# Kernel tuning notes

Hardware: AMD Instinct MI355X
Metric: run time of the kernel (lower is better)

## Reference

```python
import jax, jax.numpy as jnp
import numpy as np

B, S, D = 4, 2048, 1024


def setup_inputs() -> dict:
    key = jax.random.key(0)
    ks = jax.random.split(key, 4)
    scale = 1.0 / np.sqrt(D)
    x = jax.random.normal(ks[0], (B, S, D), dtype=jnp.float32)
    Wk = jax.random.normal(ks[1], (D, D), dtype=jnp.float32) * scale
    Wq = jax.random.normal(ks[2], (D, D), dtype=jnp.float32) * scale
    Wv = jax.random.normal(ks[3], (D, D), dtype=jnp.float32) * scale
    bk = jnp.zeros((D,), dtype=jnp.float32)
    bq = jnp.zeros((D,), dtype=jnp.float32)
    bv = jnp.zeros((D,), dtype=jnp.float32)
    return {"x": x, "Wk": Wk, "bk": bk, "Wq": Wq, "bq": bq,
            "Wv": Wv, "bv": bv, "dims": 2}


def correlated_weight(k, q, v, dims):
    # correlation between every query position and every key position,
    # scaled by sqrt(d) for numerical stability (standard correlation attn)
    d = q.shape[-1]
    scores = jnp.einsum("bqd,bkd->bqk", q, k) / jnp.sqrt(jnp.asarray(d, q.dtype))
    w = jax.nn.softmax(scores, axis=dims)          # [B, S, S]
    return jnp.einsum("bqk,bkd->bqd", w, v)        # [B, S, D]


def reference(x, Wk, bk, Wq, bq, Wv, bv, dims):
    # injected key/query/value funcs instantiated as Linear layers
    k = jnp.einsum("bsd,de->bse", x, Wk) + bk
    q = jnp.einsum("bsd,de->bse", x, Wq) + bq
    v = jnp.einsum("bsd,de->bse", x, Wv) + bv
    return correlated_weight(k, q, v, dims)
```

## Files before the change

kernel.cpp:

```cpp
#include <hip/hip_runtime.h>
#include <hip/hip_bf16.h>
#include <stdint.h>


typedef unsigned short u16;
typedef __bf16 bf16x8 __attribute__((ext_vector_type(8)));
typedef float  f32x16 __attribute__((ext_vector_type(16)));
typedef u16    u16x4  __attribute__((ext_vector_type(4)));
typedef u16    u16x8  __attribute__((ext_vector_type(8)));

__device__ __forceinline__ u16 f2bf(float f) {
  union { float f; uint32_t u; } v; v.f = f;
  uint32_t r = v.u + 0x7fffu + ((v.u >> 16) & 1u);
  return (u16)(r >> 16);
}

#define GLD_LDS16(gp, lp) __builtin_amdgcn_global_load_lds(                   \
    (const __attribute__((address_space(1))) void*)(gp),                      \
    (__attribute__((address_space(3))) void*)(lp), 16, 0, 0)


__global__ __launch_bounds__(256) void conv_x(const float* __restrict__ in,
                                              u16* __restrict__ out, int n) {
  int i = (blockIdx.x * 256 + threadIdx.x) * 4;
  if (i >= n) return;
  float4 v = *(const float4*)(in + i);
  u16x4 o; o.x = f2bf(v.x); o.y = f2bf(v.y); o.z = f2bf(v.z); o.w = f2bf(v.w);
  *(u16x4*)(out + i) = o;
}

__global__ __launch_bounds__(256) void trans_conv_w(const float* __restrict__ W,
                                                    u16* __restrict__ Wt) {
  __shared__ float t[32][33];
  int e0 = blockIdx.x * 32, d0 = blockIdx.y * 32;
  #pragma unroll
  for (int i = 0; i < 4; ++i)
    t[threadIdx.y + i * 8][threadIdx.x] =
        W[(size_t)(d0 + threadIdx.y + i * 8) * 1024 + e0 + threadIdx.x];
  __syncthreads();
  #pragma unroll
  for (int i = 0; i < 4; ++i)
    Wt[(size_t)(e0 + threadIdx.y + i * 8) * 1024 + d0 + threadIdx.x] =
        f2bf(t[threadIdx.x][threadIdx.y + i * 8]);
}

__global__ __launch_bounds__(256) void concat_bias(const float* __restrict__ bq,
                                                   const float* __restrict__ bk,
                                                   const float* __restrict__ bv,
                                                   float* __restrict__ bc) {
  int i = blockIdx.x * 256 + threadIdx.x;
  if (i >= 3072) return;
  bc[i] = (i < 1024) ? bq[i] : (i < 2048 ? bk[i - 1024] : bv[i - 2048]);
}

__global__ __launch_bounds__(256) void trans_v(const u16* __restrict__ qkv,
                                               u16* __restrict__ vT) {
  __shared__ u16 t[32][33];
  int b = blockIdx.z;
  int s0 = blockIdx.x * 32, e0 = blockIdx.y * 32;
  const u16* src = qkv + (size_t)b * 2048 * 3072 + 2048;
  u16* dst = vT + (size_t)b * 1024 * 2048;
  #pragma unroll
  for (int i = 0; i < 4; ++i)
    t[threadIdx.y + i * 8][threadIdx.x] =
        src[(size_t)(s0 + threadIdx.y + i * 8) * 3072 + e0 + threadIdx.x];
  __syncthreads();
  #pragma unroll
  for (int i = 0; i < 4; ++i)
    dst[(size_t)(e0 + threadIdx.y + i * 8) * 2048 + s0 + threadIdx.x] =
        t[threadIdx.x][threadIdx.y + i * 8];
}


template <bool OUT_BF16, bool BIAS>
__global__ __launch_bounds__(256)
void gemm_bt(const u16* __restrict__ A, int lda, long long sA,
             const u16* __restrict__ B, int ldb, long long sB,
             void* __restrict__ C, int ldc, long long sC,
             const float* __restrict__ bias, int K, float scale) {
  __shared__ u16 As[128 * 64];
  __shared__ u16 Bs[128 * 64];
  const int lane = threadIdx.x & 63;
  const int wv = threadIdx.x >> 6;

  const u16* Ab = A + (size_t)blockIdx.z * sA + (size_t)blockIdx.y * 128 * lda;
  const u16* Bb = B + (size_t)blockIdx.z * sB + (size_t)blockIdx.x * 128 * ldb;

  const int srow = lane >> 3;
  const int scol = ((lane & 7) ^ (lane >> 3)) * 8;
  const int r32 = lane & 31;
  const int half = lane >> 5;
  const int rx = lane & 7;
  const int wm = (wv >> 1) * 64;
  const int wn = (wv & 1) * 64;

  f32x16 acc[2][2];
  #pragma unroll
  for (int i = 0; i < 2; ++i)
    #pragma unroll
    for (int j = 0; j < 2; ++j) acc[i][j] = (f32x16)0.0f;

  for (int k0 = 0; k0 < K; k0 += 64) {
    #pragma unroll
    for (int i = 0; i < 4; ++i) {
      int r = wv * 32 + i * 8;
      GLD_LDS16(Ab + (size_t)(r + srow) * lda + k0 + scol, As + r * 64);
      GLD_LDS16(Bb + (size_t)(r + srow) * ldb + k0 + scol, Bs + r * 64);
    }
    __syncthreads();

    bf16x8 af[2][4], bfr[2][4];
    #pragma unroll
    for (int i = 0; i < 2; ++i)
      #pragma unroll
      for (int t = 0; t < 4; ++t) {
        int pc = ((t * 2 + half) ^ rx) * 8;
        af[i][t]  = *(const bf16x8*)(As + (wm + i * 32 + r32) * 64 + pc);
        bfr[i][t] = *(const bf16x8*)(Bs + (wn + i * 32 + r32) * 64 + pc);
      }
    #pragma unroll
    for (int i = 0; i < 2; ++i)
      #pragma unroll
      for (int j = 0; j < 2; ++j)
        #pragma unroll
        for (int t = 0; t < 4; ++t)
          acc[i][j] = __builtin_amdgcn_mfma_f32_32x32x16_bf16(
              af[i][t], bfr[j][t], acc[i][j], 0, 0, 0);
    __syncthreads();
  }

  const int ccol0 = blockIdx.x * 128 + wn + r32;
  const int crow0 = blockIdx.y * 128 + wm + 4 * half;
  u16* Cb = (u16*)C + (size_t)blockIdx.z * sC;
  float* Cf = (float*)C + (size_t)blockIdx.z * sC;
  #pragma unroll
  for (int i = 0; i < 2; ++i) {
    #pragma unroll
    for (int e = 0; e < 16; ++e) {
      int m = crow0 + i * 32 + (e & 3) + 8 * (e >> 2);
      #pragma unroll
      for (int j = 0; j < 2; ++j) {
        int n = ccol0 + j * 32;
        float v = acc[i][j][e] * scale;
        if (BIAS) v += bias[n];
        if (OUT_BF16) Cb[(size_t)m * ldc + n] = f2bf(v);
        else          Cf[(size_t)m * ldc + n] = v;
      }
    }
  }
}


__global__ __launch_bounds__(256) void softmax_rows(float* __restrict__ S) {
  __shared__ float red[4];
  const int t = threadIdx.x;
  const int lane = t & 63, wv = t >> 6;
  float* row = S + (size_t)blockIdx.x * 2048;
  const float4* rv = (const float4*)row;
  float4 a = rv[t * 2], b = rv[t * 2 + 1];
  float v[8] = {a.x, a.y, a.z, a.w, b.x, b.y, b.z, b.w};
  float m = v[0];
  #pragma unroll
  for (int j = 1; j < 8; ++j) m = fmaxf(m, v[j]);
  #pragma unroll
  for (int off = 32; off > 0; off >>= 1) m = fmaxf(m, __shfl_down(m, off));
  if (lane == 0) red[wv] = m;
  __syncthreads();
  m = fmaxf(fmaxf(red[0], red[1]), fmaxf(red[2], red[3]));
  __syncthreads();
  float e[8], s = 0.f;
  #pragma unroll
  for (int j = 0; j < 8; ++j) { e[j] = exp2f((v[j] - m) * 1.44269504f); s += e[j]; }
  #pragma unroll
  for (int off = 32; off > 0; off >>= 1) s += __shfl_down(s, off);
  if (lane == 0) red[wv] = s;
  __syncthreads();
  s = red[0] + red[1] + red[2] + red[3];
  float inv = 1.0f / s;
  u16x8 w;
  #pragma unroll
  for (int j = 0; j < 8; ++j) w[j] = f2bf(e[j] * inv);
  ((u16x8*)row)[t] = w;
}


extern "C" void kernel_launch(void* const* d_in, const int* in_sizes, int n_in,
                              void* d_out, int out_size, void* d_ws, size_t ws_size,
                              hipStream_t stream) {
  const float* x  = (const float*)d_in[0];
  const float* Wk = (const float*)d_in[1];
  const float* bk = (const float*)d_in[2];
  const float* Wq = (const float*)d_in[3];
  const float* bq = (const float*)d_in[4];
  const float* Wv = (const float*)d_in[5];
  const float* bv = (const float*)d_in[6];
  float* out = (float*)d_out;

  char* ws = (char*)d_ws;
  u16*   xb  = (u16*)(ws + 0);
  u16*   wt  = (u16*)(ws + 16777216);
  float* bc  = (float*)(ws + 23068672);
  u16*   qkv = (u16*)(ws + 23080960);
  u16*   vT  = (u16*)(ws + 73412608);
  float* sc  = (float*)(ws + 90189824);
  (void)in_sizes; (void)n_in; (void)out_size; (void)ws_size;

  conv_x<<<8192, 256, 0, stream>>>(x, xb, 8388608);
  trans_conv_w<<<dim3(32, 32), dim3(32, 8), 0, stream>>>(Wq, wt);
  trans_conv_w<<<dim3(32, 32), dim3(32, 8), 0, stream>>>(Wk, wt + 1024 * 1024);
  trans_conv_w<<<dim3(32, 32), dim3(32, 8), 0, stream>>>(Wv, wt + 2 * 1024 * 1024);
  concat_bias<<<12, 256, 0, stream>>>(bq, bk, bv, bc);

  gemm_bt<true, true><<<dim3(24, 64, 1), 256, 0, stream>>>(
      xb, 1024, 0LL, wt, 1024, 0LL, (void*)qkv, 3072, 0LL, bc, 1024, 1.0f);

  trans_v<<<dim3(64, 32, 4), dim3(32, 8), 0, stream>>>(qkv, vT);

  gemm_bt<false, false><<<dim3(16, 16, 4), 256, 0, stream>>>(
      qkv, 3072, 2048LL * 3072, qkv + 1024, 3072, 2048LL * 3072,
      (void*)sc, 2048, 2048LL * 2048, nullptr, 1024, 0.03125f);

  softmax_rows<<<8192, 256, 0, stream>>>(sc);

  gemm_bt<false, false><<<dim3(8, 16, 4), 256, 0, stream>>>(
      (const u16*)sc, 4096, 2048LL * 4096, vT, 2048, 1024LL * 2048,
      (void*)out, 1024, 2048LL * 1024, nullptr, 2048, 1.0f);
}
```

Before: 288.0 us.

## Store scores as bf16, vectorize V transpose, merge weight transposes, 8-wave PV GEMM

The QK^T GEMM now writes bf16 scores instead of fp32, so softmax reads and writes half the bytes in place. The V transpose uses 64x64 tiles with 16-byte vector loads and stores. The three weight transposes are merged into one launch. The PV GEMM uses a new 512-thread kernel so more waves cover each tile. Rounding scores to bf16 before softmax costs some accuracy.

```diff
diff --git a/kernel.cpp b/kernel.cpp
--- a/kernel.cpp
+++ b/kernel.cpp
@@ -13,6 +13,9 @@
   union { float f; uint32_t u; } v; v.f = f;
   uint32_t r = v.u + 0x7fffu + ((v.u >> 16) & 1u);
   return (u16)(r >> 16);
+}
+__device__ __forceinline__ float bf2f(u16 b) {
+  union { uint32_t u; float f; } v; v.u = (uint32_t)b << 16; return v.f;
 }
 
 #define GLD_LDS16(gp, lp) __builtin_amdgcn_global_load_lds(                   \
@@ -29,9 +32,13 @@
   *(u16x4*)(out + i) = o;
 }
 
-__global__ __launch_bounds__(256) void trans_conv_w(const float* __restrict__ W,
-                                                    u16* __restrict__ Wt) {
+__global__ __launch_bounds__(256) void trans_conv_w3(const float* __restrict__ Wq,
+                                                     const float* __restrict__ Wk,
+                                                     const float* __restrict__ Wv,
+                                                     u16* __restrict__ Wt) {
   __shared__ float t[32][33];
+  const float* W = blockIdx.z == 0 ? Wq : (blockIdx.z == 1 ? Wk : Wv);
+  u16* dst = Wt + (size_t)blockIdx.z * 1024 * 1024;
   int e0 = blockIdx.x * 32, d0 = blockIdx.y * 32;
   #pragma unroll
   for (int i = 0; i < 4; ++i)
@@ -40,7 +47,7 @@
   __syncthreads();
   #pragma unroll
   for (int i = 0; i < 4; ++i)
-    Wt[(size_t)(e0 + threadIdx.y + i * 8) * 1024 + d0 + threadIdx.x] =
+    dst[(size_t)(e0 + threadIdx.y + i * 8) * 1024 + d0 + threadIdx.x] =
         f2bf(t[threadIdx.x][threadIdx.y + i * 8]);
 }
 
@@ -55,20 +62,25 @@
 
 __global__ __launch_bounds__(256) void trans_v(const u16* __restrict__ qkv,
                                                u16* __restrict__ vT) {
-  __shared__ u16 t[32][33];
+  __shared__ u16 t[64][72];
   int b = blockIdx.z;
-  int s0 = blockIdx.x * 32, e0 = blockIdx.y * 32;
+  int s0 = blockIdx.x * 64, e0 = blockIdx.y * 64;
   const u16* src = qkv + (size_t)b * 2048 * 3072 + 2048;
   u16* dst = vT + (size_t)b * 1024 * 2048;
-  #pragma unroll
-  for (int i = 0; i < 4; ++i)
-    t[threadIdx.y + i * 8][threadIdx.x] =
-        src[(size_t)(s0 + threadIdx.y + i * 8) * 3072 + e0 + threadIdx.x];
-  __syncthreads();
-  #pragma unroll
-  for (int i = 0; i < 4; ++i)
-    dst[(size_t)(e0 + threadIdx.y + i * 8) * 2048 + s0 + threadIdx.x] =
-        t[threadIdx.x][threadIdx.y + i * 8];
+  int tx = threadIdx.x & 7, ty = threadIdx.x >> 3;
+  #pragma unroll
+  for (int rr = 0; rr < 64; rr += 32)
+    *(u16x8*)&t[ty + rr][tx * 8] =
+        *(const u16x8*)(src + (size_t)(s0 + ty + rr) * 3072 + e0 + tx * 8);
+  __syncthreads();
+  #pragma unroll
+  for (int rr = 0; rr < 64; rr += 32) {
+    int er = ty + rr;
+    u16x8 o;
+    #pragma unroll
+    for (int j = 0; j < 8; ++j) o[j] = t[tx * 8 + j][er];
+    *(u16x8*)(dst + (size_t)(e0 + er) * 2048 + s0 + tx * 8) = o;
+  }
 }
 
 
@@ -150,15 +162,78 @@
   }
 }
 
-
-__global__ __launch_bounds__(256) void softmax_rows(float* __restrict__ S) {
+__global__ __launch_bounds__(512)
+void gemm_bt8(const u16* __restrict__ A, int lda, long long sA,
+              const u16* __restrict__ B, int ldb, long long sB,
+              float* __restrict__ C, int ldc, long long sC,
+              int K, float scale) {
+  __shared__ u16 As[128 * 64];
+  __shared__ u16 Bs[128 * 64];
+  const int lane = threadIdx.x & 63;
+  const int wv = threadIdx.x >> 6;
+
+  const u16* Ab = A + (size_t)blockIdx.z * sA + (size_t)blockIdx.y * 128 * lda;
+  const u16* Bb = B + (size_t)blockIdx.z * sB + (size_t)blockIdx.x * 128 * ldb;
+
+  const int srow = lane >> 3;
+  const int scol = ((lane & 7) ^ (lane >> 3)) * 8;
+  const int r32 = lane & 31;
+  const int half = lane >> 5;
+  const int rx = lane & 7;
+  const int wm = (wv >> 2) * 64;
+  const int wn = (wv & 3) * 32;
+
+  f32x16 acc[2];
+  acc[0] = (f32x16)0.0f; acc[1] = (f32x16)0.0f;
+
+  for (int k0 = 0; k0 < K; k0 += 64) {
+    #pragma unroll
+    for (int i = 0; i < 2; ++i) {
+      int r = wv * 16 + i * 8;
+      GLD_LDS16(Ab + (size_t)(r + srow) * lda + k0 + scol, As + r * 64);
+      GLD_LDS16(Bb + (size_t)(r + srow) * ldb + k0 + scol, Bs + r * 64);
+    }
+    __syncthreads();
+
+    bf16x8 af[2][4], bfr[4];
+    #pragma unroll
+    for (int t = 0; t < 4; ++t) {
+      int pc = ((t * 2 + half) ^ rx) * 8;
+      af[0][t] = *(const bf16x8*)(As + (wm + r32) * 64 + pc);
+      af[1][t] = *(const bf16x8*)(As + (wm + 32 + r32) * 64 + pc);
+      bfr[t]   = *(const bf16x8*)(Bs + (wn + r32) * 64 + pc);
+    }
+    #pragma unroll
+    for (int i = 0; i < 2; ++i)
+      #pragma unroll
+      for (int t = 0; t < 4; ++t)
+        acc[i] = __builtin_amdgcn_mfma_f32_32x32x16_bf16(
+            af[i][t], bfr[t], acc[i], 0, 0, 0);
+    __syncthreads();
+  }
+
+  const int ccol = blockIdx.x * 128 + wn + r32;
+  const int crow0 = blockIdx.y * 128 + wm + 4 * half;
+  float* Cf = C + (size_t)blockIdx.z * sC;
+  #pragma unroll
+  for (int i = 0; i < 2; ++i)
+    #pragma unroll
+    for (int e = 0; e < 16; ++e) {
+      int m = crow0 + i * 32 + (e & 3) + 8 * (e >> 2);
+      Cf[(size_t)m * ldc + ccol] = acc[i][e] * scale;
+    }
+}
+
+
+__global__ __launch_bounds__(256) void softmax_rows(u16* __restrict__ P) {
   __shared__ float red[4];
   const int t = threadIdx.x;
   const int lane = t & 63, wv = t >> 6;
-  float* row = S + (size_t)blockIdx.x * 2048;
-  const float4* rv = (const float4*)row;
-  float4 a = rv[t * 2], b = rv[t * 2 + 1];
-  float v[8] = {a.x, a.y, a.z, a.w, b.x, b.y, b.z, b.w};
+  u16* row = P + (size_t)blockIdx.x * 2048;
+  u16x8 w = ((const u16x8*)row)[t];
+  float v[8];
+  #pragma unroll
+  for (int j = 0; j < 8; ++j) v[j] = bf2f(w[j]);
   float m = v[0];
   #pragma unroll
   for (int j = 1; j < 8; ++j) m = fmaxf(m, v[j]);
@@ -177,10 +252,10 @@
   __syncthreads();
   s = red[0] + red[1] + red[2] + red[3];
   float inv = 1.0f / s;
-  u16x8 w;
-  #pragma unroll
-  for (int j = 0; j < 8; ++j) w[j] = f2bf(e[j] * inv);
-  ((u16x8*)row)[t] = w;
+  u16x8 o;
+  #pragma unroll
+  for (int j = 0; j < 8; ++j) o[j] = f2bf(e[j] * inv);
+  ((u16x8*)row)[t] = o;
 }
 
 
@@ -202,27 +277,25 @@
   float* bc  = (float*)(ws + 23068672);
   u16*   qkv = (u16*)(ws + 23080960);
   u16*   vT  = (u16*)(ws + 73412608);
-  float* sc  = (float*)(ws + 90189824);
+  u16*   P   = (u16*)(ws + 90189824);
   (void)in_sizes; (void)n_in; (void)out_size; (void)ws_size;
 
   conv_x<<<8192, 256, 0, stream>>>(x, xb, 8388608);
-  trans_conv_w<<<dim3(32, 32), dim3(32, 8), 0, stream>>>(Wq, wt);
-  trans_conv_w<<<dim3(32, 32), dim3(32, 8), 0, stream>>>(Wk, wt + 1024 * 1024);
-  trans_conv_w<<<dim3(32, 32), dim3(32, 8), 0, stream>>>(Wv, wt + 2 * 1024 * 1024);
+  trans_conv_w3<<<dim3(32, 32, 3), dim3(32, 8), 0, stream>>>(Wq, Wk, Wv, wt);
   concat_bias<<<12, 256, 0, stream>>>(bq, bk, bv, bc);
 
   gemm_bt<true, true><<<dim3(24, 64, 1), 256, 0, stream>>>(
       xb, 1024, 0LL, wt, 1024, 0LL, (void*)qkv, 3072, 0LL, bc, 1024, 1.0f);
 
-  trans_v<<<dim3(64, 32, 4), dim3(32, 8), 0, stream>>>(qkv, vT);
-
-  gemm_bt<false, false><<<dim3(16, 16, 4), 256, 0, stream>>>(
+  trans_v<<<dim3(32, 16, 4), 256, 0, stream>>>(qkv, vT);
+
+  gemm_bt<true, false><<<dim3(16, 16, 4), 256, 0, stream>>>(
       qkv, 3072, 2048LL * 3072, qkv + 1024, 3072, 2048LL * 3072,
-      (void*)sc, 2048, 2048LL * 2048, nullptr, 1024, 0.03125f);
-
-  softmax_rows<<<8192, 256, 0, stream>>>(sc);
-
-  gemm_bt<false, false><<<dim3(8, 16, 4), 256, 0, stream>>>(
-      (const u16*)sc, 4096, 2048LL * 4096, vT, 2048, 1024LL * 2048,
-      (void*)out, 1024, 2048LL * 1024, nullptr, 2048, 1.0f);
-}
+      (void*)P, 2048, 2048LL * 2048, nullptr, 1024, 0.03125f);
+
+  softmax_rows<<<8192, 256, 0, stream>>>(P);
+
+  gemm_bt8<<<dim3(8, 16, 4), 512, 0, stream>>>(
+      P, 2048, 2048LL * 2048, vT, 2048, 1024LL * 2048,
+      out, 1024, 2048LL * 1024, 2048, 1.0f);
+}
```

After: 275.5 us. 4.3% less time.

## Fuse exp into score GEMM, drop max, defer normalization, switch to 16x16 MFMA

Applied to the files above, without the earlier changes.

The score GEMM now applies exp2 in its epilogue and writes bf16 probabilities directly, without subtracting the row max. A small rowsum kernel computes the normalizers, and the PV GEMM divides by them in its epilogue. This replaces the fp32 score matrix and the full softmax pass. The change also moves all GEMMs from 32x32 to 16x16 MFMA tiles, uses a BN=64 tile for the output GEMM, merges the three weight-transpose launches into one, and vectorizes the V transpose. Skipping the max subtraction risks overflow for large scores, and exp values are rounded to bf16 before they are summed.

```diff
diff --git a/kernel.cpp b/kernel.cpp
--- a/kernel.cpp
+++ b/kernel.cpp
@@ -5,7 +5,7 @@
 
 typedef unsigned short u16;
 typedef __bf16 bf16x8 __attribute__((ext_vector_type(8)));
-typedef float  f32x16 __attribute__((ext_vector_type(16)));
+typedef float  f32x4  __attribute__((ext_vector_type(4)));
 typedef u16    u16x4  __attribute__((ext_vector_type(4)));
 typedef u16    u16x8  __attribute__((ext_vector_type(8)));
 
@@ -13,6 +13,9 @@
   union { float f; uint32_t u; } v; v.f = f;
   uint32_t r = v.u + 0x7fffu + ((v.u >> 16) & 1u);
   return (u16)(r >> 16);
+}
+__device__ __forceinline__ float bf2f(u16 b) {
+  union { uint32_t u; float f; } v; v.u = (uint32_t)b << 16; return v.f;
 }
 
 #define GLD_LDS16(gp, lp) __builtin_amdgcn_global_load_lds(                   \
@@ -29,9 +32,13 @@
   *(u16x4*)(out + i) = o;
 }
 
-__global__ __launch_bounds__(256) void trans_conv_w(const float* __restrict__ W,
-                                                    u16* __restrict__ Wt) {
+__global__ __launch_bounds__(256) void trans_conv_w3(const float* __restrict__ Wq,
+                                                     const float* __restrict__ Wk,
+                                                     const float* __restrict__ Wv,
+                                                     u16* __restrict__ Wt) {
   __shared__ float t[32][33];
+  const float* W = blockIdx.z == 0 ? Wq : (blockIdx.z == 1 ? Wk : Wv);
+  u16* dst = Wt + (size_t)blockIdx.z * 1024 * 1024;
   int e0 = blockIdx.x * 32, d0 = blockIdx.y * 32;
   #pragma unroll
   for (int i = 0; i < 4; ++i)
@@ -40,7 +47,7 @@
   __syncthreads();
   #pragma unroll
   for (int i = 0; i < 4; ++i)
-    Wt[(size_t)(e0 + threadIdx.y + i * 8) * 1024 + d0 + threadIdx.x] =
+    dst[(size_t)(e0 + threadIdx.y + i * 8) * 1024 + d0 + threadIdx.x] =
         f2bf(t[threadIdx.x][threadIdx.y + i * 8]);
 }
 
@@ -55,94 +62,117 @@
 
 __global__ __launch_bounds__(256) void trans_v(const u16* __restrict__ qkv,
                                                u16* __restrict__ vT) {
-  __shared__ u16 t[32][33];
+  __shared__ u16 t[64][72];
   int b = blockIdx.z;
-  int s0 = blockIdx.x * 32, e0 = blockIdx.y * 32;
+  int s0 = blockIdx.x * 64, e0 = blockIdx.y * 64;
   const u16* src = qkv + (size_t)b * 2048 * 3072 + 2048;
   u16* dst = vT + (size_t)b * 1024 * 2048;
-  #pragma unroll
-  for (int i = 0; i < 4; ++i)
-    t[threadIdx.y + i * 8][threadIdx.x] =
-        src[(size_t)(s0 + threadIdx.y + i * 8) * 3072 + e0 + threadIdx.x];
+  int tx = threadIdx.x & 7, ty = threadIdx.x >> 3;
+  #pragma unroll
+  for (int rr = 0; rr < 64; rr += 32)
+    *(u16x8*)&t[ty + rr][tx * 8] =
+        *(const u16x8*)(src + (size_t)(s0 + ty + rr) * 3072 + e0 + tx * 8);
   __syncthreads();
   #pragma unroll
-  for (int i = 0; i < 4; ++i)
-    dst[(size_t)(e0 + threadIdx.y + i * 8) * 2048 + s0 + threadIdx.x] =
-        t[threadIdx.x][threadIdx.y + i * 8];
-}
-
-
-template <bool OUT_BF16, bool BIAS>
+  for (int rr = 0; rr < 64; rr += 32) {
+    int er = ty + rr;
+    u16x8 o;
+    #pragma unroll
+    for (int j = 0; j < 8; ++j) o[j] = t[tx * 8 + j][er];
+    *(u16x8*)(dst + (size_t)(e0 + er) * 2048 + s0 + tx * 8) = o;
+  }
+}
+
+
+template <int BN, bool OUT_BF16, bool BIAS, bool EXP, bool DIV>
 __global__ __launch_bounds__(256)
-void gemm_bt(const u16* __restrict__ A, int lda, long long sA,
-             const u16* __restrict__ B, int ldb, long long sB,
-             void* __restrict__ C, int ldc, long long sC,
-             const float* __restrict__ bias, int K, float scale) {
+void gemm16(const u16* __restrict__ A, int lda, long long sA,
+            const u16* __restrict__ B, int ldb, long long sB,
+            void* __restrict__ C, int ldc, long long sC,
+            const float* __restrict__ aux, int K, float scale) {
+  constexpr int NJ = BN / 32;
   __shared__ u16 As[128 * 64];
-  __shared__ u16 Bs[128 * 64];
+  __shared__ u16 Bs[BN * 64];
   const int lane = threadIdx.x & 63;
   const int wv = threadIdx.x >> 6;
 
   const u16* Ab = A + (size_t)blockIdx.z * sA + (size_t)blockIdx.y * 128 * lda;
-  const u16* Bb = B + (size_t)blockIdx.z * sB + (size_t)blockIdx.x * 128 * ldb;
+  const u16* Bb = B + (size_t)blockIdx.z * sB + (size_t)blockIdx.x * BN * ldb;
 
   const int srow = lane >> 3;
   const int scol = ((lane & 7) ^ (lane >> 3)) * 8;
-  const int r32 = lane & 31;
-  const int half = lane >> 5;
+  const int row16 = lane & 15;
+  const int quad = lane >> 4;
   const int rx = lane & 7;
   const int wm = (wv >> 1) * 64;
-  const int wn = (wv & 1) * 64;
-
-  f32x16 acc[2][2];
-  #pragma unroll
-  for (int i = 0; i < 2; ++i)
-    #pragma unroll
-    for (int j = 0; j < 2; ++j) acc[i][j] = (f32x16)0.0f;
+  const int wn = (wv & 1) * (BN / 2);
+
+  f32x4 acc[4][NJ];
+  #pragma unroll
+  for (int i = 0; i < 4; ++i)
+    #pragma unroll
+    for (int j = 0; j < NJ; ++j) acc[i][j] = (f32x4)0.0f;
 
   for (int k0 = 0; k0 < K; k0 += 64) {
     #pragma unroll
     for (int i = 0; i < 4; ++i) {
       int r = wv * 32 + i * 8;
       GLD_LDS16(Ab + (size_t)(r + srow) * lda + k0 + scol, As + r * 64);
+    }
+    #pragma unroll
+    for (int i = 0; i < BN / 32; ++i) {
+      int r = wv * (BN / 4) + i * 8;
       GLD_LDS16(Bb + (size_t)(r + srow) * ldb + k0 + scol, Bs + r * 64);
     }
     __syncthreads();
 
-    bf16x8 af[2][4], bfr[2][4];
-    #pragma unroll
-    for (int i = 0; i < 2; ++i)
-      #pragma unroll
-      for (int t = 0; t < 4; ++t) {
-        int pc = ((t * 2 + half) ^ rx) * 8;
-        af[i][t]  = *(const bf16x8*)(As + (wm + i * 32 + r32) * 64 + pc);
-        bfr[i][t] = *(const bf16x8*)(Bs + (wn + i * 32 + r32) * 64 + pc);
-      }
-    #pragma unroll
-    for (int i = 0; i < 2; ++i)
-      #pragma unroll
-      for (int j = 0; j < 2; ++j)
+    bf16x8 af[4][2], bfr[NJ][2];
+    #pragma unroll
+    for (int t = 0; t < 2; ++t) {
+      int pc = ((t * 4 + quad) ^ rx) * 8;
+      #pragma unroll
+      for (int i = 0; i < 4; ++i)
+        af[i][t] = *(const bf16x8*)(As + (wm + i * 16 + row16) * 64 + pc);
+      #pragma unroll
+      for (int j = 0; j < NJ; ++j)
+        bfr[j][t] = *(const bf16x8*)(Bs + (wn + j * 16 + row16) * 64 + pc);
+    }
+    #pragma unroll
+    for (int i = 0; i < 4; ++i)
+      #pragma unroll
+      for (int j = 0; j < NJ; ++j)
         #pragma unroll
-        for (int t = 0; t < 4; ++t)
-          acc[i][j] = __builtin_amdgcn_mfma_f32_32x32x16_bf16(
+        for (int t = 0; t < 2; ++t)
+          acc[i][j] = __builtin_amdgcn_mfma_f32_16x16x32_bf16(
               af[i][t], bfr[j][t], acc[i][j], 0, 0, 0);
     __syncthreads();
   }
 
-  const int ccol0 = blockIdx.x * 128 + wn + r32;
-  const int crow0 = blockIdx.y * 128 + wm + 4 * half;
+  const int crow0 = blockIdx.y * 128 + wm + quad * 4;
+  const int ccol0 = blockIdx.x * BN + wn + row16;
   u16* Cb = (u16*)C + (size_t)blockIdx.z * sC;
   float* Cf = (float*)C + (size_t)blockIdx.z * sC;
-  #pragma unroll
-  for (int i = 0; i < 2; ++i) {
-    #pragma unroll
-    for (int e = 0; e < 16; ++e) {
-      int m = crow0 + i * 32 + (e & 3) + 8 * (e >> 2);
-      #pragma unroll
-      for (int j = 0; j < 2; ++j) {
-        int n = ccol0 + j * 32;
-        float v = acc[i][j][e] * scale;
-        if (BIAS) v += bias[n];
+  float rl[4][4];
+  if (DIV) {
+    const float* lz = aux + (size_t)blockIdx.z * 2048;
+    #pragma unroll
+    for (int i = 0; i < 4; ++i)
+      #pragma unroll
+      for (int r = 0; r < 4; ++r)
+        rl[i][r] = 1.0f / lz[blockIdx.y * 128 + wm + quad * 4 + i * 16 + r];
+  }
+  #pragma unroll
+  for (int i = 0; i < 4; ++i) {
+    #pragma unroll
+    for (int r = 0; r < 4; ++r) {
+      int m = crow0 + i * 16 + r;
+      #pragma unroll
+      for (int j = 0; j < NJ; ++j) {
+        int n = ccol0 + j * 16;
+        float v = acc[i][j][r] * scale;
+        if (BIAS) v += aux[n];
+        if (EXP) v = exp2f(v);
+        if (DIV) v *= rl[i][r];
         if (OUT_BF16) Cb[(size_t)m * ldc + n] = f2bf(v);
         else          Cf[(size_t)m * ldc + n] = v;
       }
@@ -151,36 +181,21 @@
 }
 
 
-__global__ __launch_bounds__(256) void softmax_rows(float* __restrict__ S) {
-  __shared__ float red[4];
-  const int t = threadIdx.x;
-  const int lane = t & 63, wv = t >> 6;
-  float* row = S + (size_t)blockIdx.x * 2048;
-  const float4* rv = (const float4*)row;
-  float4 a = rv[t * 2], b = rv[t * 2 + 1];
-  float v[8] = {a.x, a.y, a.z, a.w, b.x, b.y, b.z, b.w};
-  float m = v[0];
-  #pragma unroll
-  for (int j = 1; j < 8; ++j) m = fmaxf(m, v[j]);
-  #pragma unroll
-  for (int off = 32; off > 0; off >>= 1) m = fmaxf(m, __shfl_down(m, off));
-  if (lane == 0) red[wv] = m;
-  __syncthreads();
-  m = fmaxf(fmaxf(red[0], red[1]), fmaxf(red[2], red[3]));
-  __syncthreads();
-  float e[8], s = 0.f;
-  #pragma unroll
-  for (int j = 0; j < 8; ++j) { e[j] = exp2f((v[j] - m) * 1.44269504f); s += e[j]; }
+__global__ __launch_bounds__(256) void rowsum(const u16* __restrict__ P,
+                                              float* __restrict__ l) {
+  const int lane = threadIdx.x & 63;
+  const int row = blockIdx.x * 4 + (threadIdx.x >> 6);
+  const u16* r = P + (size_t)row * 2048;
+  float s = 0.f;
+  #pragma unroll
+  for (int c = 0; c < 4; ++c) {
+    u16x8 w = *(const u16x8*)(r + c * 512 + lane * 8);
+    #pragma unroll
+    for (int j = 0; j < 8; ++j) s += bf2f(w[j]);
+  }
   #pragma unroll
   for (int off = 32; off > 0; off >>= 1) s += __shfl_down(s, off);
-  if (lane == 0) red[wv] = s;
-  __syncthreads();
-  s = red[0] + red[1] + red[2] + red[3];
-  float inv = 1.0f / s;
-  u16x8 w;
-  #pragma unroll
-  for (int j = 0; j < 8; ++j) w[j] = f2bf(e[j] * inv);
-  ((u16x8*)row)[t] = w;
+  if (lane == 0) l[row] = s;
 }
 
 
@@ -202,27 +217,26 @@
   float* bc  = (float*)(ws + 23068672);
   u16*   qkv = (u16*)(ws + 23080960);
   u16*   vT  = (u16*)(ws + 73412608);
-  float* sc  = (float*)(ws + 90189824);
+  u16*   P   = (u16*)(ws + 90189824);
+  float* l   = (float*)(ws + 123744256);
   (void)in_sizes; (void)n_in; (void)out_size; (void)ws_size;
 
   conv_x<<<8192, 256, 0, stream>>>(x, xb, 8388608);
-  trans_conv_w<<<dim3(32, 32), dim3(32, 8), 0, stream>>>(Wq, wt);
-  trans_conv_w<<<dim3(32, 32), dim3(32, 8), 0, stream>>>(Wk, wt + 1024 * 1024);
-  trans_conv_w<<<dim3(32, 32), dim3(32, 8), 0, stream>>>(Wv, wt + 2 * 1024 * 1024);
+  trans_conv_w3<<<dim3(32, 32, 3), dim3(32, 8), 0, stream>>>(Wq, Wk, Wv, wt);
   concat_bias<<<12, 256, 0, stream>>>(bq, bk, bv, bc);
 
-  gemm_bt<true, true><<<dim3(24, 64, 1), 256, 0, stream>>>(
+  gemm16<128, true, true, false, false><<<dim3(24, 64, 1), 256, 0, stream>>>(
       xb, 1024, 0LL, wt, 1024, 0LL, (void*)qkv, 3072, 0LL, bc, 1024, 1.0f);
 
-  trans_v<<<dim3(64, 32, 4), dim3(32, 8), 0, stream>>>(qkv, vT);
-
-  gemm_bt<false, false><<<dim3(16, 16, 4), 256, 0, stream>>>(
+  trans_v<<<dim3(32, 16, 4), 256, 0, stream>>>(qkv, vT);
+
+  gemm16<128, true, false, true, false><<<dim3(16, 16, 4), 256, 0, stream>>>(
       qkv, 3072, 2048LL * 3072, qkv + 1024, 3072, 2048LL * 3072,
-      (void*)sc, 2048, 2048LL * 2048, nullptr, 1024, 0.03125f);
-
-  softmax_rows<<<8192, 256, 0, stream>>>(sc);
-
-  gemm_bt<false, false><<<dim3(8, 16, 4), 256, 0, stream>>>(
-      (const u16*)sc, 4096, 2048LL * 4096, vT, 2048, 1024LL * 2048,
-      (void*)out, 1024, 2048LL * 1024, nullptr, 2048, 1.0f);
-}
+      (void*)P, 2048, 2048LL * 2048, nullptr, 1024, 0.03125f * 1.44269504f);
+
+  rowsum<<<2048, 256, 0, stream>>>(P, l);
+
+  gemm16<64, false, false, false, true><<<dim3(16, 16, 4), 256, 0, stream>>>(
+      P, 2048, 2048LL * 2048, vT, 2048, 1024LL * 2048,
+      out, 1024, 2048LL * 1024, l, 2048, 1.0f);
+}
```

Measured after the change: 290.9 us. No clear change (+1.0%).
